# Kernel tuning notes

Measured on AMD Instinct MI355X. Metric: run time of the kernel, lower is better.

The kernel has to match this reference:

```python
import jax, jax.numpy as jnp
import numpy as np

MAT_DIM = 4  # quaternion algebra vector size
EMBED_DIM = 1024
NUM_HEADS = 16
HEAD_DIM = EMBED_DIM // NUM_HEADS  # 64
SCALE = 1.0 / np.sqrt(HEAD_DIM)


def quaternion_structure():
    # C[i,j,k]: e_i * e_j = sum_k C[i,j,k] e_k, basis (1, i, j, k)
    C = np.zeros((4, 4, 4), dtype=np.float32)
    table = [
        (0, 0, 0, 1.0), (0, 1, 1, 1.0), (0, 2, 2, 1.0), (0, 3, 3, 1.0),
        (1, 0, 1, 1.0), (2, 0, 2, 1.0), (3, 0, 3, 1.0),
        (1, 1, 0, -1.0), (2, 2, 0, -1.0), (3, 3, 0, -1.0),
        (1, 2, 3, 1.0), (2, 1, 3, -1.0),
        (2, 3, 1, 1.0), (3, 2, 1, -1.0),
        (3, 1, 2, 1.0), (1, 3, 2, -1.0),
    ]
    for i, j, k, s in table:
        C[i, j, k] = s
    return jnp.asarray(C)


def algebra_linear(x, W, b, C):
    # x: [B,S,Nin,d] algebra-blocked input; W: [Nout,Nin,d]; b: [Nout,d]
    # y[b,s,o,k] = sum_{n,i,j} C[i,j,k] W[o,n,i] x[b,s,n,j] + b[o,k]
    Wm = jnp.einsum('oni,ijk->onjk', W, C)  # left-multiplication matrices
    return jnp.einsum('bsnj,onjk->bsok', x, Wm) + b


def setup_inputs() -> dict:
    key = jax.random.key(0)
    ks = jax.random.split(key, 6)
    B, S = 2, 2048
    nb = EMBED_DIM // MAT_DIM  # 256 algebra blocks
    w_std = 0.02
    inp = {
        'x': jax.random.normal(ks[0], (B, S, EMBED_DIM), dtype=jnp.float32),
        'mask': jnp.ones((1, 1, S, S), dtype=jnp.int32),
        'Wq': jax.random.normal(ks[1], (nb, nb, MAT_DIM), dtype=jnp.float32) * w_std,
        'bq': jnp.zeros((nb, MAT_DIM), dtype=jnp.float32),
        'Wk': jax.random.normal(ks[2], (nb, nb, MAT_DIM), dtype=jnp.float32) * w_std,
        'bk': jnp.zeros((nb, MAT_DIM), dtype=jnp.float32),
        'Wv': jax.random.normal(ks[3], (nb, nb, MAT_DIM), dtype=jnp.float32) * w_std,
        'bv': jnp.zeros((nb, MAT_DIM), dtype=jnp.float32),
        'Wo': jax.random.normal(ks[4], (nb, nb, MAT_DIM), dtype=jnp.float32) * w_std,
        'bo': jnp.zeros((nb, MAT_DIM), dtype=jnp.float32),
    }
    return inp


def reference(x, mask, Wq, bq, Wk, bk, Wv, bv, Wo, bo):
    C = quaternion_structure()
    B, S, E = x.shape
    xb = x.reshape(B, S, E // MAT_DIM, MAT_DIM)

    q = algebra_linear(xb, Wq, bq, C).reshape(B, S, E)
    k = algebra_linear(xb, Wk, bk, C).reshape(B, S, E)
    v = algebra_linear(xb, Wv, bv, C).reshape(B, S, E)

    def split_heads(t):  # [B,S,E] -> [B,H,S,hd]
        return t.reshape(B, S, NUM_HEADS, HEAD_DIM).transpose(0, 2, 1, 3)

    q, k, v = split_heads(q), split_heads(k), split_heads(v)

    scores = jnp.einsum('bhqd,bhkd->bhqk', q, k) * SCALE
    scores = jnp.where(mask == 0, -jnp.inf, scores)
    attn = jax.nn.softmax(scores, axis=-1)
    context = jnp.einsum('bhqk,bhkd->bhqd', attn, v)
    context = context.transpose(0, 2, 1, 3).reshape(B, S, E)

    cb = context.reshape(B, S, E // MAT_DIM, MAT_DIM)
    out = algebra_linear(cb, Wo, bo, C).reshape(B, S, E)
    return out
```

## Files before the change

kernel.cpp:

```cpp
#include <hip/hip_runtime.h>
#include <hip/hip_bf16.h>

typedef __attribute__((ext_vector_type(8))) short bf16x8;
typedef __attribute__((ext_vector_type(4))) float f32x4;
typedef __attribute__((ext_vector_type(16))) float f32x16;
typedef __attribute__((ext_vector_type(4))) unsigned short u16x4;
typedef __attribute__((ext_vector_type(4))) unsigned int u32x4;

#define LOG2E 1.4426950408889634f
#define SCLOG 0.18033688011118312f
#define EXP2(x) __builtin_amdgcn_exp2f(x)

static __device__ __forceinline__ unsigned short f2bf(float f) {
  __hip_bfloat16 h = __float2bfloat16(f);
  return __builtin_bit_cast(unsigned short, h);
}
static __device__ __forceinline__ unsigned pk2(float lo, float hg) {
  return (unsigned)f2bf(lo) | ((unsigned)f2bf(hg) << 16);
}
static __device__ __forceinline__ bf16x8 ld16(const void* p) {
  return *(const bf16x8*)p;
}
static __device__ __forceinline__ void gload16(const void* g, void* l) {
  __builtin_amdgcn_global_load_lds(
      (const __attribute__((address_space(1))) void*)g,
      (__attribute__((address_space(3))) void*)l, 16, 0, 0);
}

__global__ void cvt_bf16(const float* __restrict__ in, unsigned short* __restrict__ out)
{
  const int i = blockIdx.x * 256 + threadIdx.x;
  const float4 a = ((const float4*)in)[i];
  u16x4 o; o[0] = f2bf(a.x); o[1] = f2bf(a.y); o[2] = f2bf(a.z); o[3] = f2bf(a.w);
  ((u16x4*)out)[i] = o;
}

__global__ void expand_weights(const float* __restrict__ Wq,
                               const float* __restrict__ Wk,
                               const float* __restrict__ Wv,
                               const float* __restrict__ Wo,
                               unsigned short* __restrict__ Mqkv,
                               unsigned short* __restrict__ Mo)
{
  const int n = threadIdx.x;
  const int o = blockIdx.x;
  const int mat = blockIdx.y;
  const float* W = (mat == 0) ? Wq : (mat == 1) ? Wk : (mat == 2) ? Wv : Wo;
  unsigned short* M = (mat < 3) ? (Mqkv + (size_t)mat * 1024 * 1024) : Mo;
  const float4 w = *(const float4*)(W + ((size_t)o * 256 + n) * 4);
  const unsigned short w0 = f2bf(w.x), w1 = f2bf(w.y), w2 = f2bf(w.z), w3 = f2bf(w.w);
#define NG(u) ((unsigned short)((u) ^ 0x8000))
  u16x4 r0; r0[0] = w0;     r0[1] = NG(w1); r0[2] = NG(w2); r0[3] = NG(w3);
  u16x4 r1; r1[0] = w1;     r1[1] = w0;     r1[2] = NG(w3); r1[3] = w2;
  u16x4 r2; r2[0] = w2;     r2[1] = w3;     r2[2] = w0;     r2[3] = NG(w1);
  u16x4 r3; r3[0] = w3;     r3[1] = NG(w2); r3[2] = w1;     r3[3] = w0;
#undef NG
  unsigned short* dst = M + (size_t)(o * 4) * 1024 + n * 4;
  *(u16x4*)(dst)        = r0;
  *(u16x4*)(dst + 1024) = r1;
  *(u16x4*)(dst + 2048) = r2;
  *(u16x4*)(dst + 3072) = r3;
}

__global__ void pack_mask(const int* __restrict__ mask, unsigned long long* __restrict__ bits)
{
  const int g = blockIdx.x * 256 + threadIdx.x;
  const unsigned long long w = __ballot(mask[g] != 0);
  if ((threadIdx.x & 63) == 0) bits[g >> 6] = w;
}

template <int MODE>
__global__ __launch_bounds__(256, 3)
void gemm_bt(const unsigned short* __restrict__ A,
             const unsigned short* __restrict__ Bm,
             const float* __restrict__ bias0,
             const float* __restrict__ bias1,
             const float* __restrict__ bias2,
             unsigned short* __restrict__ out0,
             unsigned short* __restrict__ out1,
             unsigned short* __restrict__ out2,
             float* __restrict__ fout)
{
  constexpr int K = 1024;
  __shared__ unsigned short As[128 * 64];
  __shared__ unsigned short Bs[128 * 64];
  const int tid = threadIdx.x;
  const int lane = tid & 63;
  const int wave = tid >> 6;
  const int bn = blockIdx.x, bm = blockIdx.y;
  const int wm = wave >> 1, wn = wave & 1;
  const int l15 = lane & 15, l4 = lane >> 4;

  f32x4 zero4 = {0.f, 0.f, 0.f, 0.f};
  f32x4 acc[4][4];
#pragma unroll
  for (int i = 0; i < 4; ++i)
#pragma unroll
    for (int j = 0; j < 4; ++j) acc[i][j] = zero4;

  for (int kk = 0; kk < K; kk += 64) {
#pragma unroll
    for (int c = 0; c < 4; ++c) {
      const int Lb = (wave * 4 + c) * 1024;
      const int L = Lb + lane * 16;
      const int row = L >> 7;
      const int slot = (L >> 4) & 7;
      const int ss = slot ^ (row & 7);
      gload16(A + (size_t)(bm * 128 + row) * K + kk + ss * 8, (char*)As + Lb);
      gload16(Bm + (size_t)(bn * 128 + row) * K + kk + ss * 8, (char*)Bs + Lb);
    }
    __syncthreads();
#pragma unroll
    for (int ks = 0; ks < 2; ++ks) {
      bf16x8 af[4], bfr[4];
#pragma unroll
      for (int i = 0; i < 4; ++i) {
        const int ra = wm * 64 + i * 16 + l15;
        const int sa = (ks * 4 + l4) ^ (ra & 7);
        af[i] = ld16((const char*)As + ra * 128 + sa * 16);
        const int rb = wn * 64 + i * 16 + l15;
        const int sb = (ks * 4 + l4) ^ (rb & 7);
        bfr[i] = ld16((const char*)Bs + rb * 128 + sb * 16);
      }
#pragma unroll
      for (int i = 0; i < 4; ++i)
#pragma unroll
        for (int j = 0; j < 4; ++j)
          acc[i][j] = __builtin_amdgcn_mfma_f32_16x16x32_bf16(af[i], bfr[j], acc[i][j], 0, 0, 0);
    }
    __syncthreads();
  }

#pragma unroll
  for (int i = 0; i < 4; ++i) {
    const int t0 = bm * 128 + wm * 64 + i * 16 + l4 * 4;
#pragma unroll
    for (int j = 0; j < 4; ++j) {
      const int e = bn * 128 + wn * 64 + j * 16 + l15;
      f32x4 v = acc[i][j];
      if (MODE == 0) {
        const int which = e >> 10;
        const int e1 = e & 1023;
        const float* bp = (which == 0) ? bias0 : (which == 1 ? bias1 : bias2);
        const float bias = bp[e1];
        if (which == 0) {
#pragma unroll
          for (int r = 0; r < 4; ++r)
            out0[(size_t)(t0 + r) * 1024 + e1] = f2bf((v[r] + bias) * SCLOG);
        } else if (which == 1) {
#pragma unroll
          for (int r = 0; r < 4; ++r)
            out1[(size_t)(t0 + r) * 1024 + e1] = f2bf(v[r] + bias);
        } else {
          const int h = e1 >> 6, d = e1 & 63;
          const int b = t0 >> 11, s = t0 & 2047;
          u16x4 pk;
#pragma unroll
          for (int r = 0; r < 4; ++r) pk[r] = f2bf(v[r] + bias);
          *(u16x4*)&out2[((size_t)((b * 16 + h) * 64 + d)) * 2048 + s] = pk;
        }
      } else {
        const float bias = bias0[e];
#pragma unroll
        for (int r = 0; r < 4; ++r)
          fout[(size_t)(t0 + r) * 1024 + e] = v[r] + bias;
      }
    }
  }
}

__global__ __launch_bounds__(256, 3)
void attn_fwd(const unsigned short* __restrict__ q,
              const unsigned short* __restrict__ k,
              const unsigned short* __restrict__ vt,
              const unsigned long long* __restrict__ mbits,
              unsigned short* __restrict__ ctx)
{
  constexpr int S = 2048;
  __shared__ __align__(16) unsigned short Ks[2 * 4096];
  __shared__ __align__(16) unsigned short Vs[2 * 4096];

  const int bid = blockIdx.x;
  const int vb = (bid & 7) * 64 + (bid >> 3);
  const int qg = vb & 15;
  const int bh = vb >> 4;
  const int b = bh >> 4, h = bh & 15;

  const int tid = threadIdx.x, lane = tid & 63, wave = tid >> 6;
  const int l31 = lane & 31, hif = lane >> 5;
  const int sq = qg * 128 + wave * 32 + l31;
  const size_t gq = (size_t)b * S + sq;

  bf16x8 bqf[4];
#pragma unroll
  for (int s = 0; s < 4; ++s)
    bqf[s] = ld16(q + gq * 1024 + h * 64 + s * 16 + hif * 8);

  f32x16 o0 = {}, o1 = {};
  float m = -1e30f, l = 0.f;

#define STAGE(bufi, kti)                                                                  \
  {                                                                                       \
    _Pragma("unroll")                                                                     \
    for (int c = 0; c < 2; ++c) {                                                         \
      const int sl = c * 256 + tid;                                                       \
      const int row = sl >> 3;                                                            \
      const int ss = (sl & 7) ^ (row & 7);                                                \
      gload16(k + (size_t)(b * S + (kti) * 64 + row) * 1024 + h * 64 + ss * 8,            \
              (char*)Ks + (bufi) * 8192 + (c * 4 + wave) * 1024);                         \
      gload16(vt + (size_t)(bh * 64 + row) * 2048 + (kti) * 64 + ss * 8,                  \
              (char*)Vs + (bufi) * 8192 + (c * 4 + wave) * 1024);                         \
    }                                                                                     \
  }

  STAGE(0, 0);
  __syncthreads();

  int buf = 0;
  for (int kt = 0; kt < 32; ++kt) {
    const unsigned long long w = mbits[(size_t)sq * 32 + kt];
    if (kt + 1 < 32) STAGE(buf ^ 1, kt + 1);

    const char* Kb = (const char*)Ks + buf * 8192;
    f32x16 p0 = {}, p1 = {};
#pragma unroll
    for (int s = 0; s < 4; ++s) {
      const int slot = s * 2 + hif;
      const int r0 = l31, r1 = 32 + l31;
      bf16x8 a0 = ld16(Kb + r0 * 128 + ((slot ^ (r0 & 7)) << 4));
      bf16x8 a1 = ld16(Kb + r1 * 128 + ((slot ^ (r1 & 7)) << 4));
      p0 = __builtin_amdgcn_mfma_f32_32x32x16_bf16(a0, bqf[s], p0, 0, 0, 0);
      p1 = __builtin_amdgcn_mfma_f32_32x32x16_bf16(a1, bqf[s], p1, 0, 0, 0);
    }

    if (!__all(w == ~0ull)) {
#pragma unroll
      for (int c = 0; c < 16; ++c) {
        const int key = (c & 3) + 8 * (c >> 2) + 4 * hif;
        if (!((w >> key) & 1ull)) p0[c] = -INFINITY;
        if (!((w >> (key + 32)) & 1ull)) p1[c] = -INFINITY;
      }
    }

    float mx[8];
#pragma unroll
    for (int c = 0; c < 8; ++c)
      mx[c] = fmaxf(fmaxf(p0[c], p0[c + 8]), fmaxf(p1[c], p1[c + 8]));
#pragma unroll
    for (int d = 4; d; d >>= 1)
#pragma unroll
      for (int c = 0; c < d; ++c) mx[c] = fmaxf(mx[c], mx[c + d]);
    const float pm = fmaxf(mx[0], __shfl_xor(mx[0], 32, 64));

    if (pm > m + 8.f) {
      const float al = EXP2(m - pm);
      m = pm;
      l *= al;
#pragma unroll
      for (int c = 0; c < 16; ++c) { o0[c] *= al; o1[c] *= al; }
    }

#pragma unroll
    for (int c = 0; c < 16; ++c) {
      p0[c] = EXP2(p0[c] - m);
      p1[c] = EXP2(p1[c] - m);
    }
    float sm[8];
#pragma unroll
    for (int c = 0; c < 8; ++c)
      sm[c] = (p0[c] + p0[c + 8]) + (p1[c] + p1[c + 8]);
#pragma unroll
    for (int d = 4; d; d >>= 1)
#pragma unroll
      for (int c = 0; c < d; ++c) sm[c] += sm[c + d];
    l += sm[0] + __shfl_xor(sm[0], 32, 64);

    u32x4 bpw[4];
#pragma unroll
    for (int ks = 0; ks < 4; ++ks) {
      const f32x16 ps = (ks < 2) ? p0 : p1;
      const int rb2 = (ks & 1) * 8;
      unsigned X0 = pk2(ps[rb2 + 0], ps[rb2 + 1]);
      unsigned X1 = pk2(ps[rb2 + 2], ps[rb2 + 3]);
      unsigned Y0 = pk2(ps[rb2 + 4], ps[rb2 + 5]);
      unsigned Y1 = pk2(ps[rb2 + 6], ps[rb2 + 7]);
      asm("v_permlane32_swap_b32 %0, %1" : "+v"(X0), "+v"(Y0));
      asm("v_permlane32_swap_b32 %0, %1" : "+v"(X1), "+v"(Y1));
      bpw[ks][0] = X0;
      bpw[ks][1] = X1;
      bpw[ks][2] = Y0;
      bpw[ks][3] = Y1;
    }

    const char* Vb = (const char*)Vs + buf * 8192;
#pragma unroll
    for (int ks = 0; ks < 4; ++ks) {
      const bf16x8 bfrag = __builtin_bit_cast(bf16x8, bpw[ks]);
      const int slot = ks * 2 + hif;
      const int r0 = l31, r1 = 32 + l31;
      bf16x8 v0 = ld16(Vb + r0 * 128 + ((slot ^ (r0 & 7)) << 4));
      bf16x8 v1 = ld16(Vb + r1 * 128 + ((slot ^ (r1 & 7)) << 4));
      o0 = __builtin_amdgcn_mfma_f32_32x32x16_bf16(v0, bfrag, o0, 0, 0, 0);
      o1 = __builtin_amdgcn_mfma_f32_32x32x16_bf16(v1, bfrag, o1, 0, 0, 0);
    }

    __syncthreads();
    buf ^= 1;
  }
#undef STAGE

  const float inv = 1.f / l;
  unsigned short* cp = ctx + gq * 1024 + h * 64;
#pragma unroll
  for (int g = 0; g < 4; ++g) {
    u16x4 s0, s1;
#pragma unroll
    for (int t = 0; t < 4; ++t) {
      s0[t] = f2bf(o0[g * 4 + t] * inv);
      s1[t] = f2bf(o1[g * 4 + t] * inv);
    }
    *(u16x4*)(cp + g * 8 + hif * 4) = s0;
    *(u16x4*)(cp + 32 + g * 8 + hif * 4) = s1;
  }
}

extern "C" void kernel_launch(void* const* d_in, const int* in_sizes, int n_in,
                              void* d_out, int out_size, void* d_ws, size_t ws_size,
                              hipStream_t stream)
{
  const float* x  = (const float*)d_in[0];
  const int* mask = (const int*)d_in[1];
  const float* Wq = (const float*)d_in[2];
  const float* bq = (const float*)d_in[3];
  const float* Wk = (const float*)d_in[4];
  const float* bk = (const float*)d_in[5];
  const float* Wv = (const float*)d_in[6];
  const float* bv = (const float*)d_in[7];
  const float* Wo = (const float*)d_in[8];
  const float* bo = (const float*)d_in[9];

  char* ws = (char*)d_ws;
  unsigned short* Mqkv = (unsigned short*)(ws);
  unsigned short* Mo   = (unsigned short*)(ws + (6ull  << 20));
  unsigned short* qb_  = (unsigned short*)(ws + (8ull  << 20));
  unsigned short* kb_  = (unsigned short*)(ws + (16ull << 20));
  unsigned short* vtb  = (unsigned short*)(ws + (24ull << 20));
  unsigned short* ctx  = (unsigned short*)(ws + (32ull << 20));
  unsigned long long* bits = (unsigned long long*)(ws + (40ull << 20));
  unsigned short* xb   = (unsigned short*)(ws + (41ull << 20));

  cvt_bf16<<<dim3(4096), 256, 0, stream>>>(x, xb);
  expand_weights<<<dim3(256, 4), 256, 0, stream>>>(Wq, Wk, Wv, Wo, Mqkv, Mo);
  pack_mask<<<dim3(16384), 256, 0, stream>>>(mask, bits);
  gemm_bt<0><<<dim3(24, 32), 256, 0, stream>>>(xb, Mqkv, bq, bk, bv, qb_, kb_, vtb, nullptr);
  attn_fwd<<<dim3(512), 256, 0, stream>>>(qb_, kb_, vtb, bits, ctx);
  gemm_bt<1><<<dim3(8, 32), 256, 0, stream>>>(ctx, Mo, bo, bo, bo, nullptr, nullptr, nullptr,
                                              (float*)d_out);
}
```

Baseline: 129.7 us.

## Split attention over two key halves with merge kernel, fuse prep kernels

```diff
diff --git a/kernel.cpp b/kernel.cpp
--- a/kernel.cpp
+++ b/kernel.cpp
@@ -15,6 +15,10 @@
   __hip_bfloat16 h = __float2bfloat16(f);
   return __builtin_bit_cast(unsigned short, h);
 }
+static __device__ __forceinline__ float bf2f(unsigned short u) {
+  __hip_bfloat16 h = __builtin_bit_cast(__hip_bfloat16, u);
+  return __bfloat162float(h);
+}
 static __device__ __forceinline__ unsigned pk2(float lo, float hg) {
   return (unsigned)f2bf(lo) | ((unsigned)f2bf(hg) << 16);
 }
@@ -27,46 +31,48 @@
       (__attribute__((address_space(3))) void*)l, 16, 0, 0);
 }
 
-__global__ void cvt_bf16(const float* __restrict__ in, unsigned short* __restrict__ out)
+__global__ void prep(const float* __restrict__ x,
+                     const int* __restrict__ mask,
+                     const float* __restrict__ Wq,
+                     const float* __restrict__ Wk,
+                     const float* __restrict__ Wv,
+                     const float* __restrict__ Wo,
+                     unsigned short* __restrict__ xb,
+                     unsigned short* __restrict__ Mqkv,
+                     unsigned short* __restrict__ Mo,
+                     unsigned long long* __restrict__ bits)
 {
-  const int i = blockIdx.x * 256 + threadIdx.x;
-  const float4 a = ((const float4*)in)[i];
-  u16x4 o; o[0] = f2bf(a.x); o[1] = f2bf(a.y); o[2] = f2bf(a.z); o[3] = f2bf(a.w);
-  ((u16x4*)out)[i] = o;
-}
-
-__global__ void expand_weights(const float* __restrict__ Wq,
-                               const float* __restrict__ Wk,
-                               const float* __restrict__ Wv,
-                               const float* __restrict__ Wo,
-                               unsigned short* __restrict__ Mqkv,
-                               unsigned short* __restrict__ Mo)
-{
-  const int n = threadIdx.x;
-  const int o = blockIdx.x;
-  const int mat = blockIdx.y;
-  const float* W = (mat == 0) ? Wq : (mat == 1) ? Wk : (mat == 2) ? Wv : Wo;
-  unsigned short* M = (mat < 3) ? (Mqkv + (size_t)mat * 1024 * 1024) : Mo;
-  const float4 w = *(const float4*)(W + ((size_t)o * 256 + n) * 4);
-  const unsigned short w0 = f2bf(w.x), w1 = f2bf(w.y), w2 = f2bf(w.z), w3 = f2bf(w.w);
+  const int bx = blockIdx.x, tid = threadIdx.x;
+  if (bx < 16384) {
+    const int g = bx * 256 + tid;
+    const unsigned long long w = __ballot(mask[g] != 0);
+    if ((tid & 63) == 0) bits[g >> 6] = w;
+  } else if (bx < 20480) {
+    const int i = (bx - 16384) * 256 + tid;
+    const float4 a = ((const float4*)x)[i];
+    u16x4 o; o[0] = f2bf(a.x); o[1] = f2bf(a.y); o[2] = f2bf(a.z); o[3] = f2bf(a.w);
+    ((u16x4*)xb)[i] = o;
+  } else {
+    const int e = bx - 20480;
+    const int mat = e >> 8;
+    const int o = e & 255;
+    const int n = tid;
+    const float* W = (mat == 0) ? Wq : (mat == 1) ? Wk : (mat == 2) ? Wv : Wo;
+    unsigned short* M = (mat < 3) ? (Mqkv + (size_t)mat * 1024 * 1024) : Mo;
+    const float4 w = *(const float4*)(W + ((size_t)o * 256 + n) * 4);
+    const unsigned short w0 = f2bf(w.x), w1 = f2bf(w.y), w2 = f2bf(w.z), w3 = f2bf(w.w);
 #define NG(u) ((unsigned short)((u) ^ 0x8000))
-  u16x4 r0; r0[0] = w0;     r0[1] = NG(w1); r0[2] = NG(w2); r0[3] = NG(w3);
-  u16x4 r1; r1[0] = w1;     r1[1] = w0;     r1[2] = NG(w3); r1[3] = w2;
-  u16x4 r2; r2[0] = w2;     r2[1] = w3;     r2[2] = w0;     r2[3] = NG(w1);
-  u16x4 r3; r3[0] = w3;     r3[1] = NG(w2); r3[2] = w1;     r3[3] = w0;
+    u16x4 r0; r0[0] = w0;     r0[1] = NG(w1); r0[2] = NG(w2); r0[3] = NG(w3);
+    u16x4 r1; r1[0] = w1;     r1[1] = w0;     r1[2] = NG(w3); r1[3] = w2;
+    u16x4 r2; r2[0] = w2;     r2[1] = w3;     r2[2] = w0;     r2[3] = NG(w1);
+    u16x4 r3; r3[0] = w3;     r3[1] = NG(w2); r3[2] = w1;     r3[3] = w0;
 #undef NG
-  unsigned short* dst = M + (size_t)(o * 4) * 1024 + n * 4;
-  *(u16x4*)(dst)        = r0;
-  *(u16x4*)(dst + 1024) = r1;
-  *(u16x4*)(dst + 2048) = r2;
-  *(u16x4*)(dst + 3072) = r3;
-}
-
-__global__ void pack_mask(const int* __restrict__ mask, unsigned long long* __restrict__ bits)
-{
-  const int g = blockIdx.x * 256 + threadIdx.x;
-  const unsigned long long w = __ballot(mask[g] != 0);
-  if ((threadIdx.x & 63) == 0) bits[g >> 6] = w;
+    unsigned short* dst = M + (size_t)(o * 4) * 1024 + n * 4;
+    *(u16x4*)(dst)        = r0;
+    *(u16x4*)(dst + 1024) = r1;
+    *(u16x4*)(dst + 2048) = r2;
+    *(u16x4*)(dst + 3072) = r3;
+  }
 }
 
 template <int MODE>
@@ -169,21 +175,23 @@
   }
 }
 
-__global__ __launch_bounds__(256, 3)
+__global__ __launch_bounds__(256, 4)
 void attn_fwd(const unsigned short* __restrict__ q,
               const unsigned short* __restrict__ k,
               const unsigned short* __restrict__ vt,
               const unsigned long long* __restrict__ mbits,
-              unsigned short* __restrict__ ctx)
+              unsigned short* __restrict__ po,
+              float* __restrict__ sbuf)
 {
   constexpr int S = 2048;
   __shared__ __align__(16) unsigned short Ks[2 * 4096];
   __shared__ __align__(16) unsigned short Vs[2 * 4096];
 
   const int bid = blockIdx.x;
-  const int vb = (bid & 7) * 64 + (bid >> 3);
-  const int qg = vb & 15;
-  const int bh = vb >> 4;
+  const int vb = (bid & 7) * 128 + (bid >> 3);
+  const int half = vb & 1;
+  const int qg = (vb >> 1) & 15;
+  const int bh = vb >> 5;
   const int b = bh >> 4, h = bh & 15;
 
   const int tid = threadIdx.x, lane = tid & 63, wave = tid >> 6;
@@ -198,6 +206,7 @@
 
   f32x16 o0 = {}, o1 = {};
   float m = -1e30f, l = 0.f;
+  const int k0 = half * 16;
 
 #define STAGE(bufi, kti)                                                                  \
   {                                                                                       \
@@ -213,16 +222,17 @@
     }                                                                                     \
   }
 
-  STAGE(0, 0);
+  STAGE(0, k0);
   __syncthreads();
 
   int buf = 0;
-  for (int kt = 0; kt < 32; ++kt) {
+  for (int kt = k0; kt < k0 + 16; ++kt) {
     const unsigned long long w = mbits[(size_t)sq * 32 + kt];
-    if (kt + 1 < 32) STAGE(buf ^ 1, kt + 1);
+    if (kt + 1 < k0 + 16) STAGE(buf ^ 1, kt + 1);
 
     const char* Kb = (const char*)Ks + buf * 8192;
     f32x16 p0 = {}, p1 = {};
+    __builtin_amdgcn_s_setprio(1);
 #pragma unroll
     for (int s = 0; s < 4; ++s) {
       const int slot = s * 2 + hif;
@@ -232,6 +242,7 @@
       p0 = __builtin_amdgcn_mfma_f32_32x32x16_bf16(a0, bqf[s], p0, 0, 0, 0);
       p1 = __builtin_amdgcn_mfma_f32_32x32x16_bf16(a1, bqf[s], p1, 0, 0, 0);
     }
+    __builtin_amdgcn_s_setprio(0);
 
     if (!__all(w == ~0ull)) {
 #pragma unroll
@@ -293,6 +304,7 @@
     }
 
     const char* Vb = (const char*)Vs + buf * 8192;
+    __builtin_amdgcn_s_setprio(1);
 #pragma unroll
     for (int ks = 0; ks < 4; ++ks) {
       const bf16x8 bfrag = __builtin_bit_cast(bf16x8, bpw[ks]);
@@ -303,14 +315,16 @@
       o0 = __builtin_amdgcn_mfma_f32_32x32x16_bf16(v0, bfrag, o0, 0, 0, 0);
       o1 = __builtin_amdgcn_mfma_f32_32x32x16_bf16(v1, bfrag, o1, 0, 0, 0);
     }
+    __builtin_amdgcn_s_setprio(0);
 
     __syncthreads();
     buf ^= 1;
   }
 #undef STAGE
 
-  const float inv = 1.f / l;
-  unsigned short* cp = ctx + gq * 1024 + h * 64;
+  const float inv = (l > 0.f) ? 1.f / l : 0.f;
+  const float s = (l > 0.f) ? m + __log2f(l) : -1e30f;
+  unsigned short* cp = po + ((size_t)(half * 32 + bh) * 2048 + sq) * 64;
 #pragma unroll
   for (int g = 0; g < 4; ++g) {
     u16x4 s0, s1;
@@ -322,6 +336,37 @@
     *(u16x4*)(cp + g * 8 + hif * 4) = s0;
     *(u16x4*)(cp + 32 + g * 8 + hif * 4) = s1;
   }
+  if (hif == 0) sbuf[half * 65536 + bh * 2048 + sq] = s;
+}
+
+__global__ void merge_halves(const unsigned short* __restrict__ po,
+                             const float* __restrict__ sbuf,
+                             unsigned short* __restrict__ ctx)
+{
+  const int t = blockIdx.x * 256 + threadIdx.x;
+  const int row = t >> 3;
+  const int d0 = (t & 7) * 8;
+  const int bh = row >> 11, sq = row & 2047;
+  const int b = bh >> 4, h = bh & 15;
+
+  const float s0 = sbuf[row];
+  const float s1 = sbuf[65536 + row];
+  const bf16x8 a = ld16(po + (size_t)row * 64 + d0);
+  const bf16x8 c = ld16(po + 4194304 + (size_t)row * 64 + d0);
+  const float smax = fmaxf(s0, s1);
+  float w0 = EXP2(s0 - smax), w1 = EXP2(s1 - smax);
+  const float winv = 1.f / (w0 + w1);
+  w0 *= winv; w1 *= winv;
+
+  u16x4 r0, r1;
+#pragma unroll
+  for (int j = 0; j < 8; ++j) {
+    const float f = w0 * bf2f((unsigned short)a[j]) + w1 * bf2f((unsigned short)c[j]);
+    if (j < 4) r0[j] = f2bf(f); else r1[j - 4] = f2bf(f);
+  }
+  unsigned short* op = ctx + ((size_t)b * 2048 + sq) * 1024 + h * 64 + d0;
+  *(u16x4*)(op) = r0;
+  *(u16x4*)(op + 4) = r1;
 }
 
 extern "C" void kernel_launch(void* const* d_in, const int* in_sizes, int n_in,
@@ -342,18 +387,19 @@
   char* ws = (char*)d_ws;
   unsigned short* Mqkv = (unsigned short*)(ws);
   unsigned short* Mo   = (unsigned short*)(ws + (6ull  << 20));
-  unsigned short* qb_  = (unsigned short*)(ws + (8ull  << 20));
-  unsigned short* kb_  = (unsigned short*)(ws + (16ull << 20));
-  unsigned short* vtb  = (unsigned short*)(ws + (24ull << 20));
-  unsigned short* ctx  = (unsigned short*)(ws + (32ull << 20));
+  unsigned short* xb   = (unsigned short*)(ws + (8ull  << 20));
+  unsigned short* ctx  = (unsigned short*)(ws + (8ull  << 20));
+  unsigned short* qb_  = (unsigned short*)(ws + (16ull << 20));
+  unsigned short* kb_  = (unsigned short*)(ws + (24ull << 20));
+  unsigned short* vtb  = (unsigned short*)(ws + (32ull << 20));
   unsigned long long* bits = (unsigned long long*)(ws + (40ull << 20));
-  unsigned short* xb   = (unsigned short*)(ws + (41ull << 20));
-
-  cvt_bf16<<<dim3(4096), 256, 0, stream>>>(x, xb);
-  expand_weights<<<dim3(256, 4), 256, 0, stream>>>(Wq, Wk, Wv, Wo, Mqkv, Mo);
-  pack_mask<<<dim3(16384), 256, 0, stream>>>(mask, bits);
+  float* sbuf = (float*)(ws + (40ull << 20) + (512ull << 10));
+  unsigned short* po = (unsigned short*)d_out;
+
+  prep<<<dim3(21504), 256, 0, stream>>>(x, mask, Wq, Wk, Wv, Wo, xb, Mqkv, Mo, bits);
   gemm_bt<0><<<dim3(24, 32), 256, 0, stream>>>(xb, Mqkv, bq, bk, bv, qb_, kb_, vtb, nullptr);
-  attn_fwd<<<dim3(512), 256, 0, stream>>>(qb_, kb_, vtb, bits, ctx);
+  attn_fwd<<<dim3(1024), 256, 0, stream>>>(qb_, kb_, vtb, bits, po, sbuf);
+  merge_halves<<<dim3(2048), 256, 0, stream>>>(po, sbuf, ctx);
   gemm_bt<1><<<dim3(8, 32), 256, 0, stream>>>(ctx, Mo, bo, bo, bo, nullptr, nullptr, nullptr,
                                               (float*)d_out);
 }
```

Result: slower. 141.3 us (+9.0%).
